# Performance work log

Measured on AMD Instinct MI355X. Metric: run time of the kernel, lower is better.

Reference implementation:

```python
import jax, jax.numpy as jnp
import numpy as np

H = 768; P = 128; HEADS = 12; LAYERS = 3; T = 17; VD = 10
D = H // HEADS
H2 = H // 2


def _ln(x, s, b, eps=1e-5):
    m = x.mean(-1, keepdims=True)
    v = ((x - m) ** 2).mean(-1, keepdims=True)
    return (x - m) * jax.lax.rsqrt(v + eps) * s + b


def _gru_dir(x, wih, whh, bih, bhh, reverse):
    # torch nn.GRU single direction, batch_first
    if reverse:
        x = x[:, ::-1]
    xw = x @ wih.T + bih  # [B,N,3*H2]
    def step(h, xw_t):
        gh = h @ whh.T + bhh
        ir, iz, inn = jnp.split(xw_t, 3, -1)
        hr, hz, hn = jnp.split(gh, 3, -1)
        r = jax.nn.sigmoid(ir + hr)
        z = jax.nn.sigmoid(iz + hz)
        n = jnp.tanh(inn + r * hn)
        h = (1.0 - z) * n + z * h
        return h, h
    h0 = jnp.zeros((x.shape[0], whh.shape[1]), x.dtype)
    _, ys = jax.lax.scan(step, h0, jnp.swapaxes(xw, 0, 1))
    ys = jnp.swapaxes(ys, 0, 1)
    return ys[:, ::-1] if reverse else ys


def setup_inputs():
    B, EDU = 2, 95
    N = EDU + 1
    key = jax.random.key(0)
    ks = iter(jax.random.split(key, 64))
    def nrm(shape, s=0.02):
        return s * jax.random.normal(next(ks), shape, jnp.float32)
    inp = {}
    inp['sentences'] = jax.random.normal(next(ks), (B, EDU, H), jnp.float32)
    inp['speakers'] = jax.random.randint(next(ks), (B, N, N), 0, 2)
    inp['turns'] = jax.random.randint(next(ks), (B, N, N), 0, 2)
    g = jax.random.randint(next(ks), (B, N, N), 0, T)
    inp['graphs'] = jnp.tril(g, -1)  # gold graph: lower-triangular relation labels
    inp['edu_nums'] = jax.random.randint(next(ks), (B,), 60, N + 1)
    inp['root'] = jnp.zeros((H,), jnp.float32)
    for d_ in ['f', 'b']:
        inp[f'gru_wih_{d_}'] = nrm((3 * H2, H))
        inp[f'gru_whh_{d_}'] = nrm((3 * H2, H2))
        inp[f'gru_bih_{d_}'] = jnp.zeros((3 * H2,), jnp.float32)
        inp[f'gru_bhh_{d_}'] = jnp.zeros((3 * H2,), jnp.float32)
    inp['emb_speaker'] = nrm((2, P // 4), 1.0)
    inp['emb_turn'] = nrm((2, P // 4), 1.0)
    inp['emb_position'] = nrm((2 * VD + 3, P // 2), 1.0)
    inp['normal_type'] = nrm((T - 1, P), P ** -0.5)
    inp['wr'] = nrm((P, 2 * H + P)); inp['br'] = jnp.zeros((P,), jnp.float32)
    inp['wz'] = nrm((P, 2 * H + P)); inp['bz'] = jnp.zeros((P,), jnp.float32)
    inp['wc'] = nrm((P, 2 * H)); inp['bc'] = jnp.zeros((P,), jnp.float32)
    inp['wu'] = nrm((P, P)); inp['bu'] = jnp.zeros((P,), jnp.float32)
    for nm in ['wq', 'wk', 'wv', 'wo']:
        inp[nm] = nrm((H, H))
    for nm in ['bq', 'bk', 'bv', 'bo']:
        inp[nm] = jnp.zeros((H,), jnp.float32)
    inp['wsk'] = nrm((D, P)); inp['bsk'] = jnp.zeros((D,), jnp.float32)
    inp['wsv'] = nrm((D, P)); inp['bsv'] = jnp.zeros((D,), jnp.float32)
    inp['ln_s'] = jnp.ones((H,), jnp.float32); inp['ln_b'] = jnp.zeros((H,), jnp.float32)
    inp['pln_s'] = jnp.ones((P,), jnp.float32); inp['pln_b'] = jnp.zeros((P,), jnp.float32)
    CIN = 4 * H + P
    inp['link_w1'] = nrm((H, CIN)); inp['link_b1'] = jnp.zeros((H,), jnp.float32)
    inp['link_w2'] = nrm((1, H)); inp['link_b2'] = jnp.zeros((1,), jnp.float32)
    inp['lab_w1'] = nrm((H, CIN)); inp['lab_b1'] = jnp.zeros((H,), jnp.float32)
    inp['lab_w2'] = nrm((T, H)); inp['lab_b2'] = jnp.zeros((T,), jnp.float32)
    return inp


def reference(sentences, speakers, turns, graphs, edu_nums, root,
              gru_wih_f, gru_whh_f, gru_bih_f, gru_bhh_f,
              gru_wih_b, gru_whh_b, gru_bih_b, gru_bhh_b,
              emb_speaker, emb_turn, emb_position, normal_type,
              wr, br, wz, bz, wc, bc, wu, bu,
              wq, bq, wk, bk, wv, bv, wo, bo, wsk, bsk, wsv, bsv,
              ln_s, ln_b, pln_s, pln_b,
              link_w1, link_b1, link_w2, link_b2,
              lab_w1, lab_b1, lab_w2, lab_b2):
    B, EDU, _ = sentences.shape
    N = EDU + 1
    # root node + EDU embeddings -> bidirectional dialog GRU
    dialog_input = jnp.concatenate([jnp.broadcast_to(root, (B, 1, H)), sentences], axis=1)
    fw = _gru_dir(dialog_input, gru_wih_f, gru_whh_f, gru_bih_f, gru_bhh_f, False)
    bw = _gru_dir(dialog_input, gru_wih_b, gru_whh_b, gru_bih_b, gru_bhh_b, True)
    dialog_output = jnp.concatenate([fw, bw], -1)  # [B,N,H]
    # attention masking bias
    valid = jnp.arange(N)[None, :] < edu_nums[:, None]
    bias = jnp.where(valid, 0.0, -1e9)[:, None, None, :]  # [B,1,1,N]
    # constant path embedding (speaker / turn / relative position)
    idx = jnp.arange(N)
    rel = jnp.clip(idx[None, :] - idx[:, None], -VD - 1, VD + 1) + VD + 1
    pos = jnp.broadcast_to(emb_position[rel][None], (B, N, N, P // 2))
    const_path = jnp.concatenate([emb_speaker[speakers], emb_turn[turns], pos], -1)
    # gold structure path from relation labels (PathModel, padding_idx=0)
    labels = jnp.concatenate([jnp.zeros((1, P), normal_type.dtype), normal_type], 0)
    struct_path = labels[graphs + jnp.swapaxes(graphs, 1, 2)]  # [B,N,N,P]
    tril = jnp.tril(jnp.ones((N, N), bool), -1)
    triu = jnp.triu(jnp.ones((N, N), bool), 1)
    nodes = dialog_output
    scale = D ** -0.5
    for _ in range(LAYERS):
        # dns2ds: symmetrize (in-place in torch, so struct_path is replaced)
        struct_path = jnp.where(triu[None, :, :, None], jnp.swapaxes(struct_path, 1, 2), struct_path)
        paths = _ln(struct_path + const_path, pln_s, pln_b)
        q = (nodes @ wq.T + bq).reshape(B, N, HEADS, D).transpose(0, 2, 1, 3) * scale
        k = (nodes @ wk.T + bk).reshape(B, N, HEADS, D).transpose(0, 2, 1, 3)
        v = (nodes @ wv.T + bv).reshape(B, N, HEADS, D).transpose(0, 2, 1, 3)
        sk = paths @ wsk.T + bsk  # [B,N,N,D]
        sv = paths @ wsv.T + bsv
        w = (jnp.einsum('bhnd,bhmd->bhnm', q, k)
             + jnp.einsum('bhnd,bnmd->bhnm', q, sk) + bias)
        w = jax.nn.softmax(w, -1)
        out = (jnp.einsum('bhnm,bhmd->bhnd', w, v)
               + jnp.einsum('bhnm,bnmd->bhnd', w, sv))
        out = out.transpose(0, 2, 1, 3).reshape(B, N, H)
        nodes = _ln(nodes + jax.nn.relu(out @ wo.T + bo), ln_s, ln_b)
        # PathUpdateModel (GRU-style update on lower-triangular pairs)
        a = jnp.broadcast_to(nodes[:, None, :, :], (B, N, N, H))  # a[b,i,j]=nodes[b,j]
        pair = jnp.concatenate([a, jnp.swapaxes(a, 1, 2)], -1)  # [B,N,N,2H]
        rz = jnp.concatenate([pair, struct_path], -1)
        r = jax.nn.sigmoid(rz @ wr.T + br)
        z = jax.nn.sigmoid(rz @ wz.T + bz)
        u = jnp.tanh(pair @ wc.T + bc + r * (struct_path @ wu.T + bu))
        new = z * struct_path + (1.0 - z) * u
        struct_path = jnp.where(tril[None, :, :, None], new, struct_path)
    # pairwise classifier features
    multi = jnp.concatenate([dialog_input, dialog_output], -1)  # [B,N,2H]
    e = jnp.broadcast_to(multi[:, None, :, :], (B, N, N, 2 * H))
    feats = jnp.concatenate([e, jnp.swapaxes(e, 1, 2), struct_path], -1)  # [B,N,N,4H+P]
    link = (jnp.tanh(feats @ link_w1.T + link_b1) @ link_w2.T + link_b2)[..., 0]
    label = jnp.tanh(feats @ lab_w1.T + lab_b1) @ lab_w2.T + lab_b2
    return (link, label)
```

## Files before the change

### kernel.cpp

```cpp
#include <hip/hip_runtime.h>
#include <math.h>

typedef unsigned short u16;
typedef short bf16x8 __attribute__((ext_vector_type(8)));
typedef float f32x4 __attribute__((ext_vector_type(4)));


static constexpr size_t O_MULTI  = 0;
static constexpr size_t O_XWF    = O_MULTI + 294912;
static constexpr size_t O_XWB    = O_XWF   + 221184;
static constexpr size_t O_HBUF   = O_XWB   + 221184;
static constexpr size_t O_CONST  = O_HBUF  + 3072;
static constexpr size_t O_STRUCT = O_CONST + 2359296;
static constexpr size_t O_PATHS  = O_STRUCT+ 2359296;
static constexpr size_t O_NODES  = O_PATHS + 2359296;
static constexpr size_t O_QB     = O_NODES + 147456;
static constexpr size_t O_KB     = O_QB    + 147456;
static constexpr size_t O_VB     = O_KB    + 147456;
static constexpr size_t O_SKB    = O_VB    + 147456;
static constexpr size_t O_SVB    = O_SKB   + 1179648;
static constexpr size_t O_ATT    = O_SVB   + 1179648;
static constexpr size_t O_NP     = O_ATT   + 147456;
static constexpr size_t O_LAL    = O_NP    + 147456;
static constexpr size_t O_LBL    = O_LAL   + 147456;
static constexpr size_t O_LAB    = O_LBL   + 147456;
static constexpr size_t O_LBB    = O_LAB   + 147456;
static constexpr size_t O_END    = O_LBB   + 147456;

static constexpr int B_QW  = 0;
static constexpr int B_KW  = 589824;
static constexpr int B_VW  = 1179648;
static constexpr int B_OW  = 1769472;
static constexpr int B_IHF = 2359296;
static constexpr int B_IHB = 3244032;
static constexpr int B_RA  = 4128768;
static constexpr int B_RB  = 4227072;
static constexpr int B_ZA  = 4325376;
static constexpr int B_ZB  = 4423680;
static constexpr int B_CA  = 4521984;
static constexpr int B_CB  = 4620288;
static constexpr int B_CBF = 4718592;
static constexpr int B_MBF = 4980736;
static constexpr int B_NBF = 5275648;
static constexpr int B_ABF = 5423104;
static constexpr int CVT_TOT = 4980736;

static constexpr int C_WSK = 0;
static constexpr int C_WSV = 8192;
static constexpr int C_WRS = 16384;
static constexpr int C_WZS = 32768;
static constexpr int C_WU  = 49152;
static constexpr int C_W1L = 65536;
static constexpr int C_W1B = 163840;

__device__ __forceinline__ u16 f2bf(float f) {
  union { float f; unsigned u; } v; v.f = f;
  unsigned r = v.u + 0x7fff + ((v.u >> 16) & 1);
  return (u16)(r >> 16);
}

__global__ void init_kernel(const float* __restrict__ sentences,
                            const float* __restrict__ root,
                            float* __restrict__ multi, u16* __restrict__ multibf,
                            int* bar) {
  int idx = blockIdx.x * 256 + threadIdx.x;
  if (idx < 12) bar[idx * 64] = 0;
  if (idx >= 2 * 96 * 768) return;
  int c = idx % 768;
  int rem = idx / 768;
  int t = rem % 96;
  int b = rem / 96;
  float v = (t == 0) ? root[c] : sentences[((size_t)(b * 95 + (t - 1))) * 768 + c];
  size_t a = ((size_t)(b * 96 + t)) * 1536 + c;
  multi[a] = v;
  multibf[a] = f2bf(v);
}

__global__ void init_pairs_kernel(const int* __restrict__ speakers,
                                  const int* __restrict__ turns,
                                  const int* __restrict__ graphs,
                                  const float* __restrict__ emb_speaker,
                                  const float* __restrict__ emb_turn,
                                  const float* __restrict__ emb_position,
                                  const float* __restrict__ normal_type,
                                  float* __restrict__ cpath,
                                  float* __restrict__ spath) {
  int idx = blockIdx.x * 256 + threadIdx.x;
  if (idx >= 18432 * 128) return;
  int c = idx & 127;
  int p = idx >> 7;
  int j = p % 96;
  int rem = p / 96;
  int i = rem % 96;
  int b = rem / 96;
  float cv;
  if (c < 32) {
    cv = emb_speaker[speakers[p] * 32 + c];
  } else if (c < 64) {
    cv = emb_turn[turns[p] * 32 + (c - 32)];
  } else {
    int d = j - i;
    d = min(max(d, -11), 11) + 11;
    cv = emb_position[d * 64 + (c - 64)];
  }
  cpath[idx] = cv;
  int g2 = graphs[p] + graphs[(b * 96 + j) * 96 + i];
  spath[idx] = (g2 == 0) ? 0.f : normal_type[(g2 - 1) * 128 + c];
}

__global__ void cvt_weights_kernel(const float* __restrict__ wq, const float* __restrict__ wk,
                                   const float* __restrict__ wv, const float* __restrict__ wo,
                                   const float* __restrict__ wih_f, const float* __restrict__ wih_b,
                                   const float* __restrict__ wr, const float* __restrict__ wz,
                                   const float* __restrict__ wc, const float* __restrict__ wsk,
                                   const float* __restrict__ wsv, const float* __restrict__ wu,
                                   const float* __restrict__ link_w1, const float* __restrict__ lab_w1,
                                   u16* __restrict__ wbf) {
  int idx = blockIdx.x * 256 + threadIdx.x;
  if (idx >= CVT_TOT) return;
  float v;
  if (idx < B_IHF) {
    int which = idx / 589824, r = idx % 589824;
    const float* src = which == 0 ? wq : which == 1 ? wk : which == 2 ? wv : wo;
    v = src[r];
  } else if (idx < B_RA) {
    int r = idx - B_IHF;
    v = (r < 884736) ? wih_f[r] : wih_b[r - 884736];
  } else if (idx < B_CBF) {
    int r = idx - B_RA;
    int seg = r / 98304, q = r % 98304;
    int row = q / 768, c = q % 768;
    switch (seg) {
      case 0: v = wr[(size_t)row * 1664 + c]; break;
      case 1: v = wr[(size_t)row * 1664 + 768 + c]; break;
      case 2: v = wz[(size_t)row * 1664 + c]; break;
      case 3: v = wz[(size_t)row * 1664 + 768 + c]; break;
      case 4: v = wc[(size_t)row * 1536 + c]; break;
      default: v = wc[(size_t)row * 1536 + 768 + c]; break;
    }
  } else {
    int r = idx - B_CBF;
    if (r < C_WSV) v = wsk[r];
    else if (r < C_WRS) v = wsv[r - C_WSV];
    else if (r < C_WZS) { int q = r - C_WRS; v = wr[(size_t)(q >> 7) * 1664 + 1536 + (q & 127)]; }
    else if (r < C_WU)  { int q = r - C_WZS; v = wz[(size_t)(q >> 7) * 1664 + 1536 + (q & 127)]; }
    else if (r < C_W1L) v = wu[r - C_WU];
    else if (r < C_W1B) { int q = r - C_W1L; v = link_w1[(size_t)(q >> 7) * 3200 + 3072 + (q & 127)]; }
    else { int q = r - C_W1B; v = lab_w1[(size_t)(q >> 7) * 3200 + 3072 + (q & 127)]; }
  }
  wbf[idx] = f2bf(v);
}

struct BJob { const u16* W; const float* bias; float* C; };
struct BJobs { BJob j[6]; };

__global__ __launch_bounds__(256) void bgemm_kernel(const u16* __restrict__ A,
                                                    int lda, int K, int N, BJobs jobs) {
  BJob jb = jobs.j[blockIdx.z];
  int r0 = blockIdx.x * 16;
  int tid = threadIdx.x;
  int wave = tid >> 6, lane = tid & 63;
  int col = lane & 15, quad = lane >> 4;
  int c = blockIdx.y * 64 + wave * 16 + col;
  const u16* arow = A + (size_t)(r0 + col) * lda + quad * 8;
  const u16* brow = jb.W + (size_t)c * K + quad * 8;
  f32x4 acc = {0.f, 0.f, 0.f, 0.f};
  for (int k = 0; k < K; k += 32) {
    bf16x8 af = *(const bf16x8*)(arow + k);
    bf16x8 bf = *(const bf16x8*)(brow + k);
    acc = __builtin_amdgcn_mfma_f32_16x16x32_bf16(af, bf, acc, 0, 0, 0);
  }
  float bv = jb.bias ? jb.bias[c] : 0.f;
#pragma unroll
  for (int r = 0; r < 4; ++r)
    jb.C[(size_t)(r0 + quad * 4 + r) * N + c] = acc[r] + bv;
}

__device__ __forceinline__ void lnsksv_body(int blk, int tid,
                                            float* __restrict__ spath,
                                            const float* __restrict__ cpath,
                                            const float* __restrict__ pln_s,
                                            const float* __restrict__ pln_b,
                                            const u16* __restrict__ cbf,
                                            const float* __restrict__ bsk,
                                            const float* __restrict__ bsv,
                                            float* __restrict__ skb,
                                            float* __restrict__ svb,
                                            int store_upper, u16* plds) {
  int p0 = blk * 64;
  int wave = tid >> 6, lane = tid & 63;
  float pls0 = pln_s[lane], pls1 = pln_s[lane + 64];
  float plb0 = pln_b[lane], plb1 = pln_b[lane + 64];
#pragma unroll
  for (int pp = 0; pp < 8; ++pp) {
    int pl = wave * 8 + pp;
    int p = p0 + pl;
    int j = p % 96;
    int rem = p / 96;
    int i = rem % 96;
    int b = rem / 96;
    size_t self = (size_t)p * 128;
    const float* src = (i < j) ? (spath + ((size_t)((b * 96 + j) * 96 + i)) * 128)
                               : (spath + self);
    float v0 = src[lane], v1 = src[lane + 64];
    if (store_upper && i < j) {
      spath[self + lane] = v0;
      spath[self + lane + 64] = v1;
    }
    float x0 = v0 + cpath[self + lane];
    float x1 = v1 + cpath[self + lane + 64];
    float s = x0 + x1;
    for (int off = 32; off; off >>= 1) s += __shfl_xor(s, off, 64);
    float mean = s * (1.f / 128.f);
    float d0 = x0 - mean, d1 = x1 - mean;
    float vs = d0 * d0 + d1 * d1;
    for (int off = 32; off; off >>= 1) vs += __shfl_xor(vs, off, 64);
    float rstd = rsqrtf(vs * (1.f / 128.f) + 1e-5f);
    plds[pl * 136 + lane] = f2bf(d0 * rstd * pls0 + plb0);
    plds[pl * 136 + lane + 64] = f2bf(d1 * rstd * pls1 + plb1);
  }
  __syncthreads();
  int mat = wave >> 2, rowg = wave & 3;
  const u16* wb = cbf + (mat ? C_WSV : C_WSK);
  const float* bias = mat ? bsv : bsk;
  float* out = mat ? svb : skb;
  int col = lane & 15, quad = lane >> 4;
  bf16x8 afrag[4];
  const u16* arow = plds + (rowg * 16 + col) * 136 + quad * 8;
#pragma unroll
  for (int c = 0; c < 4; ++c) afrag[c] = *(const bf16x8*)(arow + 32 * c);
#pragma unroll
  for (int nt = 0; nt < 4; ++nt) {
    f32x4 acc = {0.f, 0.f, 0.f, 0.f};
    const u16* brow = wb + (size_t)(nt * 16 + col) * 128 + quad * 8;
#pragma unroll
    for (int c = 0; c < 4; ++c)
      acc = __builtin_amdgcn_mfma_f32_16x16x32_bf16(afrag[c], *(const bf16x8*)(brow + 32 * c), acc, 0, 0, 0);
    int o = nt * 16 + col;
    float bv = bias[o];
#pragma unroll
    for (int r = 0; r < 4; ++r)
      out[(size_t)(p0 + rowg * 16 + quad * 4 + r) * 64 + o] = acc[r] + bv;
  }
}

__global__ __launch_bounds__(512) void lnsksv_kernel(float* __restrict__ spath,
                                                     const float* __restrict__ cpath,
                                                     const float* __restrict__ pln_s,
                                                     const float* __restrict__ pln_b,
                                                     const u16* __restrict__ cbf,
                                                     const float* __restrict__ bsk,
                                                     const float* __restrict__ bsv,
                                                     float* __restrict__ skb,
                                                     float* __restrict__ svb,
                                                     int store_upper) {
  __shared__ u16 plds[64 * 136];
  lnsksv_body(blockIdx.x, threadIdx.x, spath, cpath, pln_s, pln_b, cbf, bsk, bsv,
              skb, svb, store_upper, plds);
}

__global__ __launch_bounds__(512) void mega_gru_kernel(
    const float* __restrict__ whh_f, const float* __restrict__ whh_b,
    const float* __restrict__ bhh_f, const float* __restrict__ bhh_b,
    const float* __restrict__ xwf, const float* __restrict__ xwb,
    float* hbuf, float* multi, u16* multibf, int* bar,
    float* __restrict__ spath, const float* __restrict__ cpath,
    const float* __restrict__ pln_s, const float* __restrict__ pln_b,
    const u16* __restrict__ cbf, const float* __restrict__ bsk,
    const float* __restrict__ bsv, float* __restrict__ skb,
    float* __restrict__ svb, const float* __restrict__ link_w1,
    const float* __restrict__ lab_w1, u16* __restrict__ l1, u16* __restrict__ b1) {
  __shared__ float hlds[768];
  __shared__ float part[3][64][2][17];
  __shared__ u16 plds[64 * 136];
  int bx = blockIdx.x;
  int tid = threadIdx.x;

  if (bx >= 300) {
    for (int idx = (bx - 300) * 512 + tid; idx < 2359296; idx += 84 * 512) {
      int half = idx / 1179648;
      int r = idx % 1179648;
      int row = r / 1536, c = r % 1536;
      size_t src = (size_t)row * 3200 + half * 1536 + c;
      l1[idx] = f2bf(link_w1[src]);
      b1[idx] = f2bf(lab_w1[src]);
    }
    return;
  }
  if (bx >= 12) {
    lnsksv_body(bx - 12, tid, spath, cpath, pln_s, pln_b, cbf, bsk, bsv, skb, svb,
                0, plds);
    return;
  }

  int dir = bx / 6;
  int sub = bx % 6;
  const float* whh = dir ? whh_b : whh_f;
  const float* bhh = dir ? bhh_b : bhh_f;
  const float* xw = dir ? xwb : xwf;
  float* hb = hbuf + (size_t)dir * 1536;
  int* flags = bar + dir * 6 * 64;

  int ks = tid >> 5;
  int ug = tid & 31;
  int hv0 = ug * 2;

  float4 wreg[6][6];
#pragma unroll
  for (int d = 0; d < 2; ++d)
#pragma unroll
    for (int g = 0; g < 3; ++g) {
      const float* wrow = whh + (size_t)(g * 384 + sub * 64 + hv0 + d) * 384 + ks * 24;
#pragma unroll
      for (int m = 0; m < 6; ++m) wreg[d * 3 + g][m] = *(const float4*)(wrow + m * 4);
    }
  float bh0 = 0.f, bh1 = 0.f, bh2 = 0.f;
  int hvC = 0, bsel = 0;
  if (tid < 128) {
    hvC = sub * 64 + (tid >> 1);
    bsel = tid & 1;
    bh0 = bhh[hvC];
    bh1 = bhh[384 + hvC];
    bh2 = bhh[768 + hvC];
  }

  for (int s = 0; s < 96; ++s) {
    int t = dir ? (95 - s) : s;
    float xr = 0.f, xz = 0.f, xn = 0.f;
    if (tid < 128) {
      const float* xrow = xw + (size_t)(bsel * 96 + t) * 1152;
      xr = xrow[hvC]; xz = xrow[384 + hvC]; xn = xrow[768 + hvC];
    }
    if (s == 0) {
      __syncthreads();
      for (int k = tid; k < 768; k += 512) hlds[k] = 0.f;
    } else {
      if (tid < 6) {
        while (__hip_atomic_load(&flags[tid * 64], __ATOMIC_RELAXED,
                                 __HIP_MEMORY_SCOPE_AGENT) < s)
          __builtin_amdgcn_s_sleep(1);
      }
      __syncthreads();
      const float* hsrc = hb + ((s - 1) & 1) * 768;
      for (int k = tid; k < 768; k += 512)
        hlds[k] = __hip_atomic_load(&hsrc[k], __ATOMIC_RELAXED, __HIP_MEMORY_SCOPE_AGENT);
    }
    __syncthreads();

    float acc[6][2];
#pragma unroll
    for (int b = 0; b < 2; ++b) {
      float4 h4[6];
      const float* hp = hlds + b * 384 + ks * 24;
#pragma unroll
      for (int m = 0; m < 6; ++m) h4[m] = *(const float4*)(hp + m * 4);
#pragma unroll
      for (int u = 0; u < 6; ++u) {
        float ssum = 0.f;
#pragma unroll
        for (int m = 0; m < 6; ++m) {
          float4 w = wreg[u][m];
          ssum += w.x * h4[m].x + w.y * h4[m].y + w.z * h4[m].z + w.w * h4[m].w;
        }
        acc[u][b] = ssum;
      }
    }
#pragma unroll
    for (int d = 0; d < 2; ++d)
#pragma unroll
      for (int g = 0; g < 3; ++g) {
        part[g][hv0 + d][0][ks] = acc[d * 3 + g][0];
        part[g][hv0 + d][1][ks] = acc[d * 3 + g][1];
      }
    __syncthreads();

    float hn = 0.f;
    if (tid < 128) {
      int hv = tid >> 1;
      float gr = bh0, gz = bh1, gn = bh2;
#pragma unroll
      for (int q = 0; q < 16; ++q) {
        gr += part[0][hv][bsel][q];
        gz += part[1][hv][bsel][q];
        gn += part[2][hv][bsel][q];
      }
      float r = 1.f / (1.f + expf(-(xr + gr)));
      float z = 1.f / (1.f + expf(-(xz + gz)));
      float n = tanhf(xn + r * gn);
      float hp = hlds[bsel * 384 + hvC];
      hn = (1.f - z) * n + z * hp;
      __hip_atomic_store(&hb[(s & 1) * 768 + bsel * 384 + hvC], hn, __ATOMIC_RELAXED,
                         __HIP_MEMORY_SCOPE_AGENT);
    }
    asm volatile("s_waitcnt vmcnt(0)" ::: "memory");
    __syncthreads();
    if (tid == 0)
      __hip_atomic_store(&flags[sub * 64], s + 1, __ATOMIC_RELAXED,
                         __HIP_MEMORY_SCOPE_AGENT);
    if (tid < 128) {
      size_t a = ((size_t)(bsel * 96 + t)) * 1536 + 768 + dir * 384 + hvC;
      multi[a] = hn;
      multibf[a] = f2bf(hn);
    }
  }
}

__global__ __launch_bounds__(256) void attn_kernel(const float* __restrict__ qb,
                                                   const float* __restrict__ kb,
                                                   const float* __restrict__ vb,
                                                   const float* __restrict__ skb,
                                                   const float* __restrict__ svb,
                                                   const int* __restrict__ edu_nums,
                                                   u16* __restrict__ attout) {
  int bi = blockIdx.x;
  int b = bi / 96;
  __shared__ float qrow[768];
  __shared__ float sc[12][100];
  int tid = threadIdx.x;
  for (int k = tid; k < 768; k += 256) qrow[k] = qb[(size_t)bi * 768 + k];
  int edun = edu_nums[b];
  __syncthreads();
  for (int task = tid; task < 12 * 96; task += 256) {
    int h = task / 96, j = task % 96;
    const float* krow = kb + ((size_t)(b * 96 + j)) * 768 + h * 64;
    const float* skrow = skb + ((size_t)(bi * 96 + j)) * 64;
    float s = 0.f;
    for (int d4 = 0; d4 < 64; d4 += 4) {
      float4 qv = *(const float4*)(qrow + h * 64 + d4);
      float4 kv = *(const float4*)(krow + d4);
      float4 sv = *(const float4*)(skrow + d4);
      s += qv.x * (kv.x + sv.x) + qv.y * (kv.y + sv.y) + qv.z * (kv.z + sv.z) +
           qv.w * (kv.w + sv.w);
    }
    s *= 0.125f;
    if (j >= edun) s -= 1e9f;
    sc[h][j] = s;
  }
  __syncthreads();
  if (tid < 12) {
    int h = tid;
    float m = -3.4e38f;
    for (int j = 0; j < 96; ++j) m = fmaxf(m, sc[h][j]);
    float sum = 0.f;
    for (int j = 0; j < 96; ++j) {
      float e = expf(sc[h][j] - m);
      sc[h][j] = e;
      sum += e;
    }
    float r = 1.f / sum;
    for (int j = 0; j < 96; ++j) sc[h][j] *= r;
  }
  __syncthreads();
  for (int o = tid; o < 768; o += 256) {
    int h = o >> 6, d = o & 63;
    float acc = 0.f;
    const float* vcol = vb + (size_t)(b * 96) * 768 + o;
    const float* svcol = svb + ((size_t)(bi * 96)) * 64 + d;
    for (int j = 0; j < 96; ++j) acc += sc[h][j] * (vcol[j * 768] + svcol[j * 64]);
    attout[(size_t)bi * 768 + o] = f2bf(acc);
  }
}

__global__ __launch_bounds__(256) void ln_nodes_kernel(const float* __restrict__ src,
                                                       int lda,
                                                       const float* __restrict__ proj,
                                                       const float* __restrict__ ln_s,
                                                       const float* __restrict__ ln_b,
                                                       float* __restrict__ nodes,
                                                       u16* __restrict__ nodesbf) {
  int row = blockIdx.x * 4 + (threadIdx.x >> 6);
  int lane = threadIdx.x & 63;
  float x[12];
  float s = 0.f;
#pragma unroll
  for (int m = 0; m < 12; ++m) {
    int e = lane + m * 64;
    float v = src[(size_t)row * lda + e] + fmaxf(proj[(size_t)row * 768 + e], 0.f);
    x[m] = v;
    s += v;
  }
  for (int off = 32; off; off >>= 1) s += __shfl_xor(s, off, 64);
  float mean = s * (1.f / 768.f);
  float vs = 0.f;
#pragma unroll
  for (int m = 0; m < 12; ++m) {
    float d = x[m] - mean;
    x[m] = d;
    vs += d * d;
  }
  for (int off = 32; off; off >>= 1) vs += __shfl_xor(vs, off, 64);
  float rstd = rsqrtf(vs * (1.f / 768.f) + 1e-5f);
#pragma unroll
  for (int m = 0; m < 12; ++m) {
    int e = lane + m * 64;
    float v = x[m] * rstd * ln_s[e] + ln_b[e];
    nodes[(size_t)row * 768 + e] = v;
    nodesbf[(size_t)row * 768 + e] = f2bf(v);
  }
}

__global__ __launch_bounds__(256) void gate_mfma_kernel(float* __restrict__ spath,
                                                        const float* __restrict__ np,
                                                        const u16* __restrict__ cbf,
                                                        const float* __restrict__ br,
                                                        const float* __restrict__ bz,
                                                        const float* __restrict__ bc,
                                                        const float* __restrict__ bu) {
  __shared__ int addrs[16], npi[16], npj[16];
  int tid = threadIdx.x;
  if (tid < 16) {
    int pid = blockIdx.x * 16 + tid;
    int b = pid / 4560;
    int t = pid % 4560;
    int i = (int)((sqrtf(8.f * (float)t + 1.f) + 1.f) * 0.5f);
    while (i * (i - 1) / 2 > t) --i;
    while ((i + 1) * i / 2 <= t) ++i;
    int j = t - i * (i - 1) / 2;
    addrs[tid] = ((b * 96 + i) * 96 + j) * 128;
    npi[tid] = (b * 96 + i) * 128;
    npj[tid] = (b * 96 + j) * 128;
  }
  __syncthreads();

  int wave = tid >> 6, lane = tid & 63;
  int col = lane & 15, quad = lane >> 4;

  bf16x8 afrag[4];
  {
    const float* arow = spath + (size_t)addrs[col] + quad * 8;
#pragma unroll
    for (int c = 0; c < 4; ++c) {
      bf16x8 f;
#pragma unroll
      for (int q = 0; q < 8; ++q) f[q] = (short)f2bf(arow[32 * c + q]);
      afrag[c] = f;
    }
  }

  const u16* wrs = cbf + C_WRS;
  const u16* wzs = cbf + C_WZS;
  const u16* wu = cbf + C_WU;

  f32x4 cr[2], cz[2], cu[2];
#pragma unroll
  for (int ct = 0; ct < 2; ++ct) {
    cr[ct] = {0.f, 0.f, 0.f, 0.f};
    cz[ct] = {0.f, 0.f, 0.f, 0.f};
    cu[ct] = {0.f, 0.f, 0.f, 0.f};
    int o0 = wave * 32 + ct * 16;
    const u16* br_ = wrs + (size_t)(o0 + col) * 128 + quad * 8;
    const u16* bz_ = wzs + (size_t)(o0 + col) * 128 + quad * 8;
    const u16* bu_ = wu + (size_t)(o0 + col) * 128 + quad * 8;
#pragma unroll
    for (int c = 0; c < 4; ++c) {
      cr[ct] = __builtin_amdgcn_mfma_f32_16x16x32_bf16(afrag[c], *(const bf16x8*)(br_ + 32 * c), cr[ct], 0, 0, 0);
      cz[ct] = __builtin_amdgcn_mfma_f32_16x16x32_bf16(afrag[c], *(const bf16x8*)(bz_ + 32 * c), cz[ct], 0, 0, 0);
      cu[ct] = __builtin_amdgcn_mfma_f32_16x16x32_bf16(afrag[c], *(const bf16x8*)(bu_ + 32 * c), cu[ct], 0, 0, 0);
    }
  }

#pragma unroll
  for (int ct = 0; ct < 2; ++ct) {
    int o = wave * 32 + ct * 16 + col;
    float brv = br[o], bzv = bz[o], bcv = bc[o], buv = bu[o];
#pragma unroll
    for (int r4 = 0; r4 < 4; ++r4) {
      int m = quad * 4 + r4;
      int sa = addrs[m] + o;
      float so = spath[sa];
      float nra = np[0 * 24576 + npj[m] + o];
      float nrb = np[1 * 24576 + npi[m] + o];
      float nza = np[2 * 24576 + npj[m] + o];
      float nzb = np[3 * 24576 + npi[m] + o];
      float nca = np[4 * 24576 + npj[m] + o];
      float ncb = np[5 * 24576 + npi[m] + o];
      float r = 1.f / (1.f + expf(-(cr[ct][r4] + nra + nrb + brv)));
      float z = 1.f / (1.f + expf(-(cz[ct][r4] + nza + nzb + bzv)));
      float u = tanhf(nca + ncb + bcv + r * (cu[ct][r4] + buv));
      spath[sa] = z * so + (1.f - z) * u;
    }
  }
}

__global__ __launch_bounds__(256) void final_mfma_kernel(
    const float* __restrict__ spath, const u16* __restrict__ cbf,
    const float* __restrict__ LAl, const float* __restrict__ LBl,
    const float* __restrict__ LAb, const float* __restrict__ LBb,
    const float* __restrict__ w2l, const float* __restrict__ w2b,
    const float* __restrict__ b2l, const float* __restrict__ b2b,
    float* __restrict__ outlink, float* __restrict__ outlab) {
  const u16* w1l = cbf + C_W1L;
  const u16* w1b = cbf + C_W1B;
  int p0 = blockIdx.x * 16;
  int j0 = p0 % 96;
  int rem = p0 / 96;
  int i = rem % 96;
  int b = rem / 96;
  int tid = threadIdx.x;
  int wave = tid >> 6;
  int lane = tid & 63;
  int col = lane & 15;
  int quad = lane >> 4;

  __shared__ float redl[4][16];
  __shared__ float red[4][16][17];

  bf16x8 afrag[4];
  {
    const float* arow = spath + (size_t)(p0 + col) * 128 + quad * 8;
#pragma unroll
    for (int c = 0; c < 4; ++c) {
      bf16x8 f;
#pragma unroll
      for (int q = 0; q < 8; ++q) f[q] = (short)f2bf(arow[32 * c + q]);
      afrag[c] = f;
    }
  }

  float lacc[4] = {0.f, 0.f, 0.f, 0.f};
  float at[4][17];
#pragma unroll
  for (int r = 0; r < 4; ++r)
#pragma unroll
    for (int t = 0; t < 17; ++t) at[r][t] = 0.f;

  const float* LBl_row = LBl + (size_t)(b * 96 + i) * 768;
  const float* LBb_row = LBb + (size_t)(b * 96 + i) * 768;

  for (int nt = wave; nt < 48; nt += 4) {
    int o0 = nt * 16;
    f32x4 c = {0.f, 0.f, 0.f, 0.f};
    const u16* brow = w1l + (size_t)(o0 + col) * 128 + quad * 8;
#pragma unroll
    for (int cc = 0; cc < 4; ++cc) {
      bf16x8 bf = *(const bf16x8*)(brow + 32 * cc);
      c = __builtin_amdgcn_mfma_f32_16x16x32_bf16(afrag[cc], bf, c, 0, 0, 0);
    }
    int o = o0 + col;
    float lb = LBl_row[o];
    float w2 = w2l[o];
#pragma unroll
    for (int r = 0; r < 4; ++r) {
      int m = quad * 4 + r;
      float la = LAl[(size_t)(b * 96 + j0 + m) * 768 + o];
      float h = tanhf(c[r] + la + lb);
      lacc[r] += h * w2;
    }
  }

  for (int nt = wave; nt < 48; nt += 4) {
    int o0 = nt * 16;
    f32x4 c = {0.f, 0.f, 0.f, 0.f};
    const u16* brow = w1b + (size_t)(o0 + col) * 128 + quad * 8;
#pragma unroll
    for (int cc = 0; cc < 4; ++cc) {
      bf16x8 bf = *(const bf16x8*)(brow + 32 * cc);
      c = __builtin_amdgcn_mfma_f32_16x16x32_bf16(afrag[cc], bf, c, 0, 0, 0);
    }
    int o = o0 + col;
    float lb = LBb_row[o];
#pragma unroll
    for (int r = 0; r < 4; ++r) {
      int m = quad * 4 + r;
      float la = LAb[(size_t)(b * 96 + j0 + m) * 768 + o];
      float h = tanhf(c[r] + la + lb);
#pragma unroll
      for (int t = 0; t < 17; ++t) at[r][t] += h * w2b[t * 768 + o];
    }
  }

#pragma unroll
  for (int r = 0; r < 4; ++r) {
    lacc[r] += __shfl_xor(lacc[r], 1, 64);
    lacc[r] += __shfl_xor(lacc[r], 2, 64);
    lacc[r] += __shfl_xor(lacc[r], 4, 64);
    lacc[r] += __shfl_xor(lacc[r], 8, 64);
#pragma unroll
    for (int t = 0; t < 17; ++t) {
      at[r][t] += __shfl_xor(at[r][t], 1, 64);
      at[r][t] += __shfl_xor(at[r][t], 2, 64);
      at[r][t] += __shfl_xor(at[r][t], 4, 64);
      at[r][t] += __shfl_xor(at[r][t], 8, 64);
    }
  }
  if (col == 0) {
#pragma unroll
    for (int r = 0; r < 4; ++r) {
      int m = quad * 4 + r;
      redl[wave][m] = lacc[r];
#pragma unroll
      for (int t = 0; t < 17; ++t) red[wave][m][t] = at[r][t];
    }
  }
  __syncthreads();
  if (tid < 16) {
    float s = redl[0][tid] + redl[1][tid] + redl[2][tid] + redl[3][tid];
    outlink[(size_t)((b * 96 + i) * 96) + j0 + tid] = s + b2l[0];
  }
  for (int task = tid; task < 16 * 17; task += 256) {
    int m = task / 17, t = task % 17;
    float s = red[0][m][t] + red[1][m][t] + red[2][m][t] + red[3][m][t];
    outlab[((size_t)((b * 96 + i) * 96) + j0 + m) * 17 + t] = s + b2b[t];
  }
}

extern "C" void kernel_launch(void* const* d_in, const int* in_sizes, int n_in,
                              void* d_out, int out_size, void* d_ws, size_t ws_size,
                              hipStream_t stream) {
  (void)in_sizes; (void)n_in; (void)out_size; (void)ws_size;
  const float* sentences = (const float*)d_in[0];
  const int* speakers = (const int*)d_in[1];
  const int* turns = (const int*)d_in[2];
  const int* graphs = (const int*)d_in[3];
  const int* edu_nums = (const int*)d_in[4];
  const float* root = (const float*)d_in[5];
  const float* wih_f = (const float*)d_in[6];
  const float* whh_f = (const float*)d_in[7];
  const float* bih_f = (const float*)d_in[8];
  const float* bhh_f = (const float*)d_in[9];
  const float* wih_b = (const float*)d_in[10];
  const float* whh_b = (const float*)d_in[11];
  const float* bih_b = (const float*)d_in[12];
  const float* bhh_b = (const float*)d_in[13];
  const float* emb_speaker = (const float*)d_in[14];
  const float* emb_turn = (const float*)d_in[15];
  const float* emb_position = (const float*)d_in[16];
  const float* normal_type = (const float*)d_in[17];
  const float* wr = (const float*)d_in[18];
  const float* br = (const float*)d_in[19];
  const float* wz = (const float*)d_in[20];
  const float* bz = (const float*)d_in[21];
  const float* wc = (const float*)d_in[22];
  const float* bc = (const float*)d_in[23];
  const float* wu = (const float*)d_in[24];
  const float* bu = (const float*)d_in[25];
  const float* wq = (const float*)d_in[26];
  const float* wk = (const float*)d_in[27];
  const float* wv = (const float*)d_in[28];
  const float* wo = (const float*)d_in[29];
  const float* bq = (const float*)d_in[30];
  const float* bk = (const float*)d_in[31];
  const float* bv = (const float*)d_in[32];
  const float* bo = (const float*)d_in[33];
  const float* wsk = (const float*)d_in[34];
  const float* bsk = (const float*)d_in[35];
  const float* wsv = (const float*)d_in[36];
  const float* bsv = (const float*)d_in[37];
  const float* ln_s = (const float*)d_in[38];
  const float* ln_b = (const float*)d_in[39];
  const float* pln_s = (const float*)d_in[40];
  const float* pln_b = (const float*)d_in[41];
  const float* link_w1 = (const float*)d_in[42];
  const float* link_b1 = (const float*)d_in[43];
  const float* link_w2 = (const float*)d_in[44];
  const float* link_b2 = (const float*)d_in[45];
  const float* lab_w1 = (const float*)d_in[46];
  const float* lab_b1 = (const float*)d_in[47];
  const float* lab_w2 = (const float*)d_in[48];
  const float* lab_b2 = (const float*)d_in[49];

  int* bar = (int*)d_ws;
  float* W = (float*)((char*)d_ws + 4096);
  float* multi = W + O_MULTI;
  float* xwf = W + O_XWF;
  float* xwb = W + O_XWB;
  float* hbuf = W + O_HBUF;
  float* cpath = W + O_CONST;
  float* spath = W + O_STRUCT;
  float* nodes = W + O_NODES;
  float* qb = W + O_QB;
  float* kb = W + O_KB;
  float* vb = W + O_VB;
  float* skb = W + O_SKB;
  float* svb = W + O_SVB;
  float* np = W + O_NP;
  float* LAl = W + O_LAL;
  float* LBl = W + O_LBL;
  float* LAb = W + O_LAB;
  float* LBb = W + O_LBB;
  u16* l1 = (u16*)(W + O_PATHS);
  u16* b1 = l1 + 2359296;
  u16* wbf = (u16*)(W + O_END);
  u16* cbf = wbf + B_CBF;
  u16* multibf = wbf + B_MBF;
  u16* nodesbf = wbf + B_NBF;
  u16* attoutbf = wbf + B_ABF;
  float* outlink = (float*)d_out;
  float* outlab = (float*)d_out + 18432;

  init_kernel<<<576, 256, 0, stream>>>(sentences, root, multi, multibf, bar);

  cvt_weights_kernel<<<19456, 256, 0, stream>>>(wq, wk, wv, wo, wih_f, wih_b, wr, wz,
                                                wc, wsk, wsv, wu, link_w1, lab_w1, wbf);

  {
    BJobs j{};
    j.j[0] = {wbf + B_IHF, bih_f, xwf};
    j.j[1] = {wbf + B_IHB, bih_b, xwb};
    bgemm_kernel<<<dim3(12, 18, 2), 256, 0, stream>>>(multibf, 1536, 768, 1152, j);
  }

  init_pairs_kernel<<<9216, 256, 0, stream>>>(speakers, turns, graphs, emb_speaker,
                                              emb_turn, emb_position, normal_type,
                                              cpath, spath);

  mega_gru_kernel<<<384, 512, 0, stream>>>(whh_f, whh_b, bhh_f, bhh_b, xwf, xwb,
                                           hbuf, multi, multibf, bar, spath, cpath,
                                           pln_s, pln_b, cbf, bsk, bsv, skb, svb,
                                           link_w1, lab_w1, l1, b1);

  for (int layer = 0; layer < 3; ++layer) {
    const u16* nsrcbf = (layer == 0) ? (multibf + 768) : nodesbf;
    int nlda = (layer == 0) ? 1536 : 768;
    const float* nsrc = (layer == 0) ? (multi + 768) : nodes;

    if (layer > 0)
      lnsksv_kernel<<<288, 512, 0, stream>>>(spath, cpath, pln_s, pln_b, cbf, bsk,
                                             bsv, skb, svb, layer == 2 ? 1 : 0);

    {
      BJobs j{};
      j.j[0] = {wbf + B_QW, bq, qb};
      j.j[1] = {wbf + B_KW, bk, kb};
      j.j[2] = {wbf + B_VW, bv, vb};
      bgemm_kernel<<<dim3(12, 12, 3), 256, 0, stream>>>(nsrcbf, nlda, 768, 768, j);
    }

    attn_kernel<<<192, 256, 0, stream>>>(qb, kb, vb, skb, svb, edu_nums, attoutbf);

    {
      BJobs j{};
      j.j[0] = {wbf + B_OW, bo, qb};
      bgemm_kernel<<<dim3(12, 12, 1), 256, 0, stream>>>(attoutbf, 768, 768, 768, j);
    }

    ln_nodes_kernel<<<48, 256, 0, stream>>>(nsrc, nlda, qb, ln_s, ln_b, nodes,
                                            nodesbf);

    {
      BJobs j{};
      j.j[0] = {wbf + B_RA, nullptr, np + 0 * 24576};
      j.j[1] = {wbf + B_RB, nullptr, np + 1 * 24576};
      j.j[2] = {wbf + B_ZA, nullptr, np + 2 * 24576};
      j.j[3] = {wbf + B_ZB, nullptr, np + 3 * 24576};
      j.j[4] = {wbf + B_CA, nullptr, np + 4 * 24576};
      j.j[5] = {wbf + B_CB, nullptr, np + 5 * 24576};
      bgemm_kernel<<<dim3(12, 2, 6), 256, 0, stream>>>(nodesbf, 768, 768, 128, j);
    }

    gate_mfma_kernel<<<570, 256, 0, stream>>>(spath, np, cbf, br, bz, bc, bu);
  }

  {
    BJobs j{};
    j.j[0] = {l1, link_b1, LAl};
    j.j[1] = {l1 + 1179648, nullptr, LBl};
    j.j[2] = {b1, lab_b1, LAb};
    j.j[3] = {b1 + 1179648, nullptr, LBb};
    bgemm_kernel<<<dim3(12, 12, 4), 256, 0, stream>>>(multibf, 1536, 1536, 768, j);
  }

  final_mfma_kernel<<<1152, 256, 0, stream>>>(spath, cbf, LAl, LBl, LAb, LBb,
                                              link_w2, lab_w2, link_b2, lab_b2,
                                              outlink, outlab);
}
```

Before: 991.8 us.

## Fuse setup, pair-init and per-layer GEMMs into fewer kernel launches

Merges the weight conversion and input init into one setup kernel that converts four elements per thread. Folds the pair embedding init into the GRU kernel's path-LN blocks and fuses the per-layer LN/SK/SV with the QKV GEMM. The link/label first-layer GEMM now runs inside layer 1's combined launch instead of a separate final launch. Also parallelizes the attention softmax across 16 lanes per head instead of one thread. The aim is to cut launch count and serial tails, at the cost of heterogeneous blocks that may balance poorly.

```diff
diff --git a/kernel.cpp b/kernel.cpp
--- a/kernel.cpp
+++ b/kernel.cpp
@@ -59,11 +59,60 @@
   return (u16)(r >> 16);
 }
 
-__global__ void init_kernel(const float* __restrict__ sentences,
-                            const float* __restrict__ root,
-                            float* __restrict__ multi, u16* __restrict__ multibf,
-                            int* bar) {
-  int idx = blockIdx.x * 256 + threadIdx.x;
+__global__ void setup_kernel(const float* __restrict__ wq, const float* __restrict__ wk,
+                             const float* __restrict__ wv, const float* __restrict__ wo,
+                             const float* __restrict__ wih_f, const float* __restrict__ wih_b,
+                             const float* __restrict__ wr, const float* __restrict__ wz,
+                             const float* __restrict__ wc, const float* __restrict__ wsk,
+                             const float* __restrict__ wsv, const float* __restrict__ wu,
+                             const float* __restrict__ link_w1, const float* __restrict__ lab_w1,
+                             u16* __restrict__ wbf,
+                             const float* __restrict__ sentences,
+                             const float* __restrict__ root,
+                             float* __restrict__ multi, u16* __restrict__ multibf,
+                             int* bar) {
+  int bx = blockIdx.x;
+  int tid = threadIdx.x;
+  if (bx < 4864) {
+    int g = bx * 256 + tid;
+#pragma unroll
+    for (int q = 0; q < 4; ++q) {
+      int idx = g * 4 + q;
+      float v;
+      if (idx < B_IHF) {
+        int which = idx / 589824, r = idx % 589824;
+        const float* src = which == 0 ? wq : which == 1 ? wk : which == 2 ? wv : wo;
+        v = src[r];
+      } else if (idx < B_RA) {
+        int r = idx - B_IHF;
+        v = (r < 884736) ? wih_f[r] : wih_b[r - 884736];
+      } else if (idx < B_CBF) {
+        int r = idx - B_RA;
+        int seg = r / 98304, qq = r % 98304;
+        int row = qq / 768, c = qq % 768;
+        switch (seg) {
+          case 0: v = wr[(size_t)row * 1664 + c]; break;
+          case 1: v = wr[(size_t)row * 1664 + 768 + c]; break;
+          case 2: v = wz[(size_t)row * 1664 + c]; break;
+          case 3: v = wz[(size_t)row * 1664 + 768 + c]; break;
+          case 4: v = wc[(size_t)row * 1536 + c]; break;
+          default: v = wc[(size_t)row * 1536 + 768 + c]; break;
+        }
+      } else {
+        int r = idx - B_CBF;
+        if (r < C_WSV) v = wsk[r];
+        else if (r < C_WRS) v = wsv[r - C_WSV];
+        else if (r < C_WZS) { int qr = r - C_WRS; v = wr[(size_t)(qr >> 7) * 1664 + 1536 + (qr & 127)]; }
+        else if (r < C_WU)  { int qr = r - C_WZS; v = wz[(size_t)(qr >> 7) * 1664 + 1536 + (qr & 127)]; }
+        else if (r < C_W1L) v = wu[r - C_WU];
+        else if (r < C_W1B) { int qr = r - C_W1L; v = link_w1[(size_t)(qr >> 7) * 3200 + 3072 + (qr & 127)]; }
+        else { int qr = r - C_W1B; v = lab_w1[(size_t)(qr >> 7) * 3200 + 3072 + (qr & 127)]; }
+      }
+      wbf[idx] = f2bf(v);
+    }
+    return;
+  }
+  int idx = (bx - 4864) * 256 + tid;
   if (idx < 12) bar[idx * 64] = 0;
   if (idx >= 2 * 96 * 768) return;
   int c = idx % 768;
@@ -74,81 +123,6 @@
   size_t a = ((size_t)(b * 96 + t)) * 1536 + c;
   multi[a] = v;
   multibf[a] = f2bf(v);
-}
-
-__global__ void init_pairs_kernel(const int* __restrict__ speakers,
-                                  const int* __restrict__ turns,
-                                  const int* __restrict__ graphs,
-                                  const float* __restrict__ emb_speaker,
-                                  const float* __restrict__ emb_turn,
-                                  const float* __restrict__ emb_position,
-                                  const float* __restrict__ normal_type,
-                                  float* __restrict__ cpath,
-                                  float* __restrict__ spath) {
-  int idx = blockIdx.x * 256 + threadIdx.x;
-  if (idx >= 18432 * 128) return;
-  int c = idx & 127;
-  int p = idx >> 7;
-  int j = p % 96;
-  int rem = p / 96;
-  int i = rem % 96;
-  int b = rem / 96;
-  float cv;
-  if (c < 32) {
-    cv = emb_speaker[speakers[p] * 32 + c];
-  } else if (c < 64) {
-    cv = emb_turn[turns[p] * 32 + (c - 32)];
-  } else {
-    int d = j - i;
-    d = min(max(d, -11), 11) + 11;
-    cv = emb_position[d * 64 + (c - 64)];
-  }
-  cpath[idx] = cv;
-  int g2 = graphs[p] + graphs[(b * 96 + j) * 96 + i];
-  spath[idx] = (g2 == 0) ? 0.f : normal_type[(g2 - 1) * 128 + c];
-}
-
-__global__ void cvt_weights_kernel(const float* __restrict__ wq, const float* __restrict__ wk,
-                                   const float* __restrict__ wv, const float* __restrict__ wo,
-                                   const float* __restrict__ wih_f, const float* __restrict__ wih_b,
-                                   const float* __restrict__ wr, const float* __restrict__ wz,
-                                   const float* __restrict__ wc, const float* __restrict__ wsk,
-                                   const float* __restrict__ wsv, const float* __restrict__ wu,
-                                   const float* __restrict__ link_w1, const float* __restrict__ lab_w1,
-                                   u16* __restrict__ wbf) {
-  int idx = blockIdx.x * 256 + threadIdx.x;
-  if (idx >= CVT_TOT) return;
-  float v;
-  if (idx < B_IHF) {
-    int which = idx / 589824, r = idx % 589824;
-    const float* src = which == 0 ? wq : which == 1 ? wk : which == 2 ? wv : wo;
-    v = src[r];
-  } else if (idx < B_RA) {
-    int r = idx - B_IHF;
-    v = (r < 884736) ? wih_f[r] : wih_b[r - 884736];
-  } else if (idx < B_CBF) {
-    int r = idx - B_RA;
-    int seg = r / 98304, q = r % 98304;
-    int row = q / 768, c = q % 768;
-    switch (seg) {
-      case 0: v = wr[(size_t)row * 1664 + c]; break;
-      case 1: v = wr[(size_t)row * 1664 + 768 + c]; break;
-      case 2: v = wz[(size_t)row * 1664 + c]; break;
-      case 3: v = wz[(size_t)row * 1664 + 768 + c]; break;
-      case 4: v = wc[(size_t)row * 1536 + c]; break;
-      default: v = wc[(size_t)row * 1536 + 768 + c]; break;
-    }
-  } else {
-    int r = idx - B_CBF;
-    if (r < C_WSV) v = wsk[r];
-    else if (r < C_WRS) v = wsv[r - C_WSV];
-    else if (r < C_WZS) { int q = r - C_WRS; v = wr[(size_t)(q >> 7) * 1664 + 1536 + (q & 127)]; }
-    else if (r < C_WU)  { int q = r - C_WZS; v = wz[(size_t)(q >> 7) * 1664 + 1536 + (q & 127)]; }
-    else if (r < C_W1L) v = wu[r - C_WU];
-    else if (r < C_W1B) { int q = r - C_W1L; v = link_w1[(size_t)(q >> 7) * 3200 + 3072 + (q & 127)]; }
-    else { int q = r - C_W1B; v = lab_w1[(size_t)(q >> 7) * 3200 + 3072 + (q & 127)]; }
-  }
-  wbf[idx] = f2bf(v);
 }
 
 struct BJob { const u16* W; const float* bias; float* C; };
@@ -176,6 +150,60 @@
     jb.C[(size_t)(r0 + quad * 4 + r) * N + c] = acc[r] + bv;
 }
 
+__device__ __forceinline__ void bgemm512(const u16* __restrict__ A, int lda, int K,
+                                         int N, const u16* __restrict__ Wt,
+                                         const float* __restrict__ bias,
+                                         float* __restrict__ C, int rowblk,
+                                         int colblk, int tid) {
+  int wave = tid >> 6, lane = tid & 63;
+  int col = lane & 15, quad = lane >> 4;
+  int c = colblk * 128 + wave * 16 + col;
+  int r0 = rowblk * 16;
+  const u16* arow = A + (size_t)(r0 + col) * lda + quad * 8;
+  const u16* brow = Wt + (size_t)c * K + quad * 8;
+  f32x4 acc = {0.f, 0.f, 0.f, 0.f};
+  for (int k = 0; k < K; k += 32) {
+    bf16x8 af = *(const bf16x8*)(arow + k);
+    bf16x8 bf = *(const bf16x8*)(brow + k);
+    acc = __builtin_amdgcn_mfma_f32_16x16x32_bf16(af, bf, acc, 0, 0, 0);
+  }
+  float bv = bias ? bias[c] : 0.f;
+#pragma unroll
+  for (int r = 0; r < 4; ++r)
+    C[(size_t)(r0 + quad * 4 + r) * N + c] = acc[r] + bv;
+}
+
+__device__ __forceinline__ void sksv_tail(int tid, int p0, const u16* plds,
+                                          const u16* __restrict__ cbf,
+                                          const float* __restrict__ bsk,
+                                          const float* __restrict__ bsv,
+                                          float* __restrict__ skb,
+                                          float* __restrict__ svb) {
+  int wave = tid >> 6, lane = tid & 63;
+  int mat = wave >> 2, rowg = wave & 3;
+  const u16* wb = cbf + (mat ? C_WSV : C_WSK);
+  const float* bias = mat ? bsv : bsk;
+  float* out = mat ? svb : skb;
+  int col = lane & 15, quad = lane >> 4;
+  bf16x8 afrag[4];
+  const u16* arow = plds + (rowg * 16 + col) * 136 + quad * 8;
+#pragma unroll
+  for (int c = 0; c < 4; ++c) afrag[c] = *(const bf16x8*)(arow + 32 * c);
+#pragma unroll
+  for (int nt = 0; nt < 4; ++nt) {
+    f32x4 acc = {0.f, 0.f, 0.f, 0.f};
+    const u16* brow = wb + (size_t)(nt * 16 + col) * 128 + quad * 8;
+#pragma unroll
+    for (int c = 0; c < 4; ++c)
+      acc = __builtin_amdgcn_mfma_f32_16x16x32_bf16(afrag[c], *(const bf16x8*)(brow + 32 * c), acc, 0, 0, 0);
+    int o = nt * 16 + col;
+    float bv = bias[o];
+#pragma unroll
+    for (int r = 0; r < 4; ++r)
+      out[(size_t)(p0 + rowg * 16 + quad * 4 + r) * 64 + o] = acc[r] + bv;
+  }
+}
+
 __device__ __forceinline__ void lnsksv_body(int blk, int tid,
                                             float* __restrict__ spath,
                                             const float* __restrict__ cpath,
@@ -220,43 +248,64 @@
     plds[pl * 136 + lane + 64] = f2bf(d1 * rstd * pls1 + plb1);
   }
   __syncthreads();
-  int mat = wave >> 2, rowg = wave & 3;
-  const u16* wb = cbf + (mat ? C_WSV : C_WSK);
-  const float* bias = mat ? bsv : bsk;
-  float* out = mat ? svb : skb;
-  int col = lane & 15, quad = lane >> 4;
-  bf16x8 afrag[4];
-  const u16* arow = plds + (rowg * 16 + col) * 136 + quad * 8;
-#pragma unroll
-  for (int c = 0; c < 4; ++c) afrag[c] = *(const bf16x8*)(arow + 32 * c);
-#pragma unroll
-  for (int nt = 0; nt < 4; ++nt) {
-    f32x4 acc = {0.f, 0.f, 0.f, 0.f};
-    const u16* brow = wb + (size_t)(nt * 16 + col) * 128 + quad * 8;
-#pragma unroll
-    for (int c = 0; c < 4; ++c)
-      acc = __builtin_amdgcn_mfma_f32_16x16x32_bf16(afrag[c], *(const bf16x8*)(brow + 32 * c), acc, 0, 0, 0);
-    int o = nt * 16 + col;
-    float bv = bias[o];
-#pragma unroll
-    for (int r = 0; r < 4; ++r)
-      out[(size_t)(p0 + rowg * 16 + quad * 4 + r) * 64 + o] = acc[r] + bv;
-  }
-}
-
-__global__ __launch_bounds__(512) void lnsksv_kernel(float* __restrict__ spath,
-                                                     const float* __restrict__ cpath,
-                                                     const float* __restrict__ pln_s,
-                                                     const float* __restrict__ pln_b,
-                                                     const u16* __restrict__ cbf,
-                                                     const float* __restrict__ bsk,
-                                                     const float* __restrict__ bsv,
-                                                     float* __restrict__ skb,
-                                                     float* __restrict__ svb,
-                                                     int store_upper) {
-  __shared__ u16 plds[64 * 136];
-  lnsksv_body(blockIdx.x, threadIdx.x, spath, cpath, pln_s, pln_b, cbf, bsk, bsv,
-              skb, svb, store_upper, plds);
+  sksv_tail(tid, p0, plds, cbf, bsk, bsv, skb, svb);
+}
+
+__device__ __forceinline__ void lnsksv0_body(int blk, int tid,
+                                             const int* __restrict__ speakers,
+                                             const int* __restrict__ turns,
+                                             const int* __restrict__ graphs,
+                                             const float* __restrict__ emb_speaker,
+                                             const float* __restrict__ emb_turn,
+                                             const float* __restrict__ emb_position,
+                                             const float* __restrict__ normal_type,
+                                             float* __restrict__ cpath,
+                                             float* __restrict__ spath,
+                                             const float* __restrict__ pln_s,
+                                             const float* __restrict__ pln_b,
+                                             const u16* __restrict__ cbf,
+                                             const float* __restrict__ bsk,
+                                             const float* __restrict__ bsv,
+                                             float* __restrict__ skb,
+                                             float* __restrict__ svb, u16* plds) {
+  int p0 = blk * 64;
+  int wave = tid >> 6, lane = tid & 63;
+  float pls0 = pln_s[lane], pls1 = pln_s[lane + 64];
+  float plb0 = pln_b[lane], plb1 = pln_b[lane + 64];
+#pragma unroll
+  for (int pp = 0; pp < 8; ++pp) {
+    int pl = wave * 8 + pp;
+    int p = p0 + pl;
+    int j = p % 96;
+    int rem = p / 96;
+    int i = rem % 96;
+    int b = rem / 96;
+    int sp = speakers[p], tn = turns[p];
+    int g2 = graphs[p] + graphs[(b * 96 + j) * 96 + i];
+    int d = min(max(j - i, -11), 11) + 11;
+    float cv0 = (lane < 32) ? emb_speaker[sp * 32 + lane] : emb_turn[tn * 32 + lane - 32];
+    float cv1 = emb_position[d * 64 + lane];
+    float s0 = (g2 == 0) ? 0.f : normal_type[(g2 - 1) * 128 + lane];
+    float s1 = (g2 == 0) ? 0.f : normal_type[(g2 - 1) * 128 + 64 + lane];
+    size_t self = (size_t)p * 128;
+    cpath[self + lane] = cv0;
+    cpath[self + lane + 64] = cv1;
+    spath[self + lane] = s0;
+    spath[self + lane + 64] = s1;
+    float x0 = s0 + cv0;
+    float x1 = s1 + cv1;
+    float s = x0 + x1;
+    for (int off = 32; off; off >>= 1) s += __shfl_xor(s, off, 64);
+    float mean = s * (1.f / 128.f);
+    float d0 = x0 - mean, d1 = x1 - mean;
+    float vs = d0 * d0 + d1 * d1;
+    for (int off = 32; off; off >>= 1) vs += __shfl_xor(vs, off, 64);
+    float rstd = rsqrtf(vs * (1.f / 128.f) + 1e-5f);
+    plds[pl * 136 + lane] = f2bf(d0 * rstd * pls0 + plb0);
+    plds[pl * 136 + lane + 64] = f2bf(d1 * rstd * pls1 + plb1);
+  }
+  __syncthreads();
+  sksv_tail(tid, p0, plds, cbf, bsk, bsv, skb, svb);
 }
 
 __global__ __launch_bounds__(512) void mega_gru_kernel(
@@ -264,7 +313,11 @@
     const float* __restrict__ bhh_f, const float* __restrict__ bhh_b,
     const float* __restrict__ xwf, const float* __restrict__ xwb,
     float* hbuf, float* multi, u16* multibf, int* bar,
-    float* __restrict__ spath, const float* __restrict__ cpath,
+    const int* __restrict__ speakers, const int* __restrict__ turns,
+    const int* __restrict__ graphs, const float* __restrict__ emb_speaker,
+    const float* __restrict__ emb_turn, const float* __restrict__ emb_position,
+    const float* __restrict__ normal_type, float* __restrict__ cpath,
+    float* __restrict__ spath,
     const float* __restrict__ pln_s, const float* __restrict__ pln_b,
     const u16* __restrict__ cbf, const float* __restrict__ bsk,
     const float* __restrict__ bsv, float* __restrict__ skb,
@@ -288,8 +341,9 @@
     return;
   }
   if (bx >= 12) {
-    lnsksv_body(bx - 12, tid, spath, cpath, pln_s, pln_b, cbf, bsk, bsv, skb, svb,
-                0, plds);
+    lnsksv0_body(bx - 12, tid, speakers, turns, graphs, emb_speaker, emb_turn,
+                 emb_position, normal_type, cpath, spath, pln_s, pln_b, cbf, bsk,
+                 bsv, skb, svb, plds);
     return;
   }
 
@@ -403,6 +457,48 @@
       multibf[a] = f2bf(hn);
     }
   }
+}
+
+__global__ __launch_bounds__(512) void layerA_kernel(
+    float* __restrict__ spath, const float* __restrict__ cpath,
+    const float* __restrict__ pln_s, const float* __restrict__ pln_b,
+    const u16* __restrict__ cbf, const float* __restrict__ bsk,
+    const float* __restrict__ bsv, float* __restrict__ skb,
+    float* __restrict__ svb, int store_upper,
+    const u16* __restrict__ nodesbf, const u16* __restrict__ wbf,
+    const float* __restrict__ bq, const float* __restrict__ bk,
+    const float* __restrict__ bv, float* __restrict__ qb, float* __restrict__ kb,
+    float* __restrict__ vb, const u16* __restrict__ multibf,
+    const u16* __restrict__ l1, const u16* __restrict__ b1,
+    const float* __restrict__ link_b1, const float* __restrict__ lab_b1,
+    float* __restrict__ LAl, float* __restrict__ LBl, float* __restrict__ LAb,
+    float* __restrict__ LBb) {
+  __shared__ u16 plds[64 * 136];
+  int bx = blockIdx.x;
+  int tid = threadIdx.x;
+  if (bx < 288) {
+    lnsksv_body(bx, tid, spath, cpath, pln_s, pln_b, cbf, bsk, bsv, skb, svb,
+                store_upper, plds);
+    return;
+  }
+  int bxl = bx - 288;
+  if (bxl < 216) {
+    int job = bxl / 72, rem = bxl % 72;
+    int rowblk = rem % 12, colblk = rem / 12;
+    const u16* Wt = wbf + (job == 0 ? B_QW : job == 1 ? B_KW : B_VW);
+    const float* bias = job == 0 ? bq : job == 1 ? bk : bv;
+    float* C = job == 0 ? qb : job == 1 ? kb : vb;
+    bgemm512(nodesbf, 768, 768, 768, Wt, bias, C, rowblk, colblk, tid);
+    return;
+  }
+  bxl -= 216;
+  int job = bxl / 72, rem = bxl % 72;
+  int rowblk = rem % 12, colblk = rem / 12;
+  const u16* Wt = job == 0 ? l1 : job == 1 ? l1 + 1179648 : job == 2 ? b1
+                                                                     : b1 + 1179648;
+  const float* bias = job == 0 ? link_b1 : job == 2 ? lab_b1 : nullptr;
+  float* C = job == 0 ? LAl : job == 1 ? LBl : job == 2 ? LAb : LBb;
+  bgemm512(multibf, 1536, 1536, 768, Wt, bias, C, rowblk, colblk, tid);
 }
 
 __global__ __launch_bounds__(256) void attn_kernel(const float* __restrict__ qb,
@@ -437,18 +533,26 @@
     sc[h][j] = s;
   }
   __syncthreads();
-  if (tid < 12) {
-    int h = tid;
+  if (tid < 192) {
+    int h = tid >> 4, s5 = tid & 15;
     float m = -3.4e38f;
-    for (int j = 0; j < 96; ++j) m = fmaxf(m, sc[h][j]);
+    for (int j = s5; j < 96; j += 16) m = fmaxf(m, sc[h][j]);
+    m = fmaxf(m, __shfl_xor(m, 1, 64));
+    m = fmaxf(m, __shfl_xor(m, 2, 64));
+    m = fmaxf(m, __shfl_xor(m, 4, 64));
+    m = fmaxf(m, __shfl_xor(m, 8, 64));
     float sum = 0.f;
-    for (int j = 0; j < 96; ++j) {
+    for (int j = s5; j < 96; j += 16) {
       float e = expf(sc[h][j] - m);
       sc[h][j] = e;
       sum += e;
     }
+    sum += __shfl_xor(sum, 1, 64);
+    sum += __shfl_xor(sum, 2, 64);
+    sum += __shfl_xor(sum, 4, 64);
+    sum += __shfl_xor(sum, 8, 64);
     float r = 1.f / sum;
-    for (int j = 0; j < 96; ++j) sc[h][j] *= r;
+    for (int j = s5; j < 96; j += 16) sc[h][j] *= r;
   }
   __syncthreads();
   for (int o = tid; o < 768; o += 256) {
@@ -788,10 +892,9 @@
   float* outlink = (float*)d_out;
   float* outlab = (float*)d_out + 18432;
 
-  init_kernel<<<576, 256, 0, stream>>>(sentences, root, multi, multibf, bar);
-
-  cvt_weights_kernel<<<19456, 256, 0, stream>>>(wq, wk, wv, wo, wih_f, wih_b, wr, wz,
-                                                wc, wsk, wsv, wu, link_w1, lab_w1, wbf);
+  setup_kernel<<<5440, 256, 0, stream>>>(wq, wk, wv, wo, wih_f, wih_b, wr, wz, wc,
+                                         wsk, wsv, wu, link_w1, lab_w1, wbf,
+                                         sentences, root, multi, multibf, bar);
 
   {
     BJobs j{};
@@ -800,12 +903,10 @@
     bgemm_kernel<<<dim3(12, 18, 2), 256, 0, stream>>>(multibf, 1536, 768, 1152, j);
   }
 
-  init_pairs_kernel<<<9216, 256, 0, stream>>>(speakers, turns, graphs, emb_speaker,
-                                              emb_turn, emb_position, normal_type,
-                                              cpath, spath);
-
   mega_gru_kernel<<<384, 512, 0, stream>>>(whh_f, whh_b, bhh_f, bhh_b, xwf, xwb,
-                                           hbuf, multi, multibf, bar, spath, cpath,
+                                           hbuf, multi, multibf, bar, speakers,
+                                           turns, graphs, emb_speaker, emb_turn,
+                                           emb_position, normal_type, cpath, spath,
                                            pln_s, pln_b, cbf, bsk, bsv, skb, svb,
                                            link_w1, lab_w1, l1, b1);
 
@@ -814,16 +915,18 @@
     int nlda = (layer == 0) ? 1536 : 768;
     const float* nsrc = (layer == 0) ? (multi + 768) : nodes;
 
-    if (layer > 0)
-      lnsksv_kernel<<<288, 512, 0, stream>>>(spath, cpath, pln_s, pln_b, cbf, bsk,
-                                             bsv, skb, svb, layer == 2 ? 1 : 0);
-
-    {
+    if (layer == 0) {
       BJobs j{};
       j.j[0] = {wbf + B_QW, bq, qb};
       j.j[1] = {wbf + B_KW, bk, kb};
       j.j[2] = {wbf + B_VW, bv, vb};
       bgemm_kernel<<<dim3(12, 12, 3), 256, 0, stream>>>(nsrcbf, nlda, 768, 768, j);
+    } else {
+      int has_lab = (layer == 1);
+      layerA_kernel<<<288 + 216 + (has_lab ? 288 : 0), 512, 0, stream>>>(
+          spath, cpath, pln_s, pln_b, cbf, bsk, bsv, skb, svb,
+          (layer == 2) ? 1 : 0, nodesbf, wbf, bq, bk, bv, qb, kb, vb, multibf, l1,
+          b1, link_b1, lab_b1, LAl, LBl, LAb, LBb);
     }
 
     attn_kernel<<<192, 256, 0, stream>>>(qb, kb, vb, skb, svb, edu_nums, attoutbf);
@@ -851,15 +954,6 @@
     gate_mfma_kernel<<<570, 256, 0, stream>>>(spath, np, cbf, br, bz, bc, bu);
   }
 
-  {
-    BJobs j{};
-    j.j[0] = {l1, link_b1, LAl};
-    j.j[1] = {l1 + 1179648, nullptr, LBl};
-    j.j[2] = {b1, lab_b1, LAb};
-    j.j[3] = {b1 + 1179648, nullptr, LBb};
-    bgemm_kernel<<<dim3(12, 12, 4), 256, 0, stream>>>(multibf, 1536, 1536, 768, j);
-  }
-
   final_mfma_kernel<<<1152, 256, 0, stream>>>(spath, cbf, LAl, LBl, LAb, LBb,
                                               link_w2, lab_w2, link_b2, lab_b2,
                                               outlink, outlab);
```

Result: faster. 953.9 us (-3.8%).
